# Kernel optimization log

Hardware: AMD Instinct MI355X
Metric: run time of the kernel (lower is better)

Reference implementation:

```python
import jax, jax.numpy as jnp
import numpy as np

N_NODES = 50000
N_RAND_EDGES = 800000  # plus N_NODES self-loop edges appended in setup
IN_FEATS, N_HIDDEN, N_CLASSES = 128, 64, 64


def setup_inputs() -> dict:
    key = jax.random.key(0)
    kf, ks, kd, k1, k2, k3 = jax.random.split(key, 6)
    features = jax.random.normal(kf, (N_NODES, IN_FEATS), dtype=jnp.float32)
    src = jax.random.randint(ks, (N_RAND_EDGES,), 0, N_NODES, dtype=jnp.int32)
    dst = jax.random.randint(kd, (N_RAND_EDGES,), 0, N_NODES, dtype=jnp.int32)
    # dgl.add_self_loop: append (i, i) for every node
    loop = jnp.arange(N_NODES, dtype=jnp.int32)
    src = jnp.concatenate([src, loop])
    dst = jnp.concatenate([dst, loop])

    def glorot(k, fan_in, fan_out):
        lim = jnp.sqrt(6.0 / (fan_in + fan_out)).astype(jnp.float32)
        return jax.random.uniform(k, (fan_in, fan_out), jnp.float32, -lim, lim)

    return {
        "features": features, "src": src, "dst": dst,
        "W1": glorot(k1, IN_FEATS, N_HIDDEN), "b1": jnp.zeros((N_HIDDEN,), jnp.float32),
        "W2": glorot(k2, N_HIDDEN, N_HIDDEN), "b2": jnp.zeros((N_HIDDEN,), jnp.float32),
        "W3": glorot(k3, N_HIDDEN, N_CLASSES), "b3": jnp.zeros((N_CLASSES,), jnp.float32),
    }


def _graph_conv(x, W, b, src, dst, norm_src_e, norm_dst_n, n_nodes):
    """DGL GraphConv, norm='both': D_dst^{-1/2} A D_src^{-1/2} X W + b, then relu."""
    if W.shape[0] > W.shape[1]:  # mult by W first when it shrinks the feature dim
        x = x @ W
        m = x[src] * norm_src_e[:, None]                      # [E, out]
        h = jax.ops.segment_sum(m, dst, num_segments=n_nodes)  # [N, out]
        h = h * norm_dst_n[:, None]
    else:
        m = x[src] * norm_src_e[:, None]                      # [E, in]
        h = jax.ops.segment_sum(m, dst, num_segments=n_nodes)  # [N, in]
        h = (h * norm_dst_n[:, None]) @ W
    return jax.nn.relu(h + b)


def reference(features, src, dst, W1, b1, W2, b2, W3, b3):
    n = features.shape[0]
    ones = jnp.ones(src.shape[0], dtype=features.dtype)
    out_deg = jax.ops.segment_sum(ones, src, num_segments=n)
    in_deg = jax.ops.segment_sum(ones, dst, num_segments=n)
    norm_out = jnp.where(out_deg > 0, jax.lax.rsqrt(jnp.maximum(out_deg, 1.0)), 0.0)
    norm_in = jnp.where(in_deg > 0, jax.lax.rsqrt(jnp.maximum(in_deg, 1.0)), 0.0)
    norm_src_e = norm_out[src]  # per-edge source normalization

    h1 = _graph_conv(features, W1, b1, src, dst, norm_src_e, norm_in, n)
    h2 = _graph_conv(h1, W2, b2, src, dst, norm_src_e, norm_in, n)
    h3 = _graph_conv(h2, W3, b3, src, dst, norm_src_e, norm_in, n)
    # JumpingKnowledge mode='max': elementwise max over stacked layer outputs
    return jnp.max(jnp.stack([h1, h2, h3], axis=0), axis=0)
```

## Files before the change

### kernel.cpp

```cpp
#include <hip/hip_runtime.h>

typedef _Float16 h16;
typedef __attribute__((ext_vector_type(4))) _Float16 half4;
typedef __attribute__((ext_vector_type(8))) _Float16 half8;
typedef __attribute__((ext_vector_type(8))) float float8;

#define RANGES 8
#define PPR    64
#define HTHREADS 1024
#define BINS   6400
#define HALF   (BINS / 2)
#define HWORDS (BINS)
#define NSEG   100

__global__ __launch_bounds__(HTHREADS) void hist_kernel(const int* __restrict__ src,
                                                        const int* __restrict__ dst,
                                                        int* __restrict__ partial, int E) {
  __shared__ int h[HWORDS];
  const int r = blockIdx.x >> 6;
  const int c = blockIdx.x & 63;
  for (int i = threadIdx.x; i < HWORDS; i += HTHREADS) h[i] = 0;
  __syncthreads();
  const int lo = r * BINS;
  const int chunk = (E + PPR - 1) / PPR;
  const int e0 = c * chunk;
  const int e1 = min(E, e0 + chunk);
  for (int e = e0 + threadIdx.x; e < e1; e += HTHREADS) {
    int s = src[e] - lo;
    if ((unsigned)s < (unsigned)BINS) atomicAdd(&h[s >> 1], 1 << ((s & 1) * 16));
    int d = dst[e] - lo;
    if ((unsigned)d < (unsigned)BINS) atomicAdd(&h[HALF + (d >> 1)], 1 << ((d & 1) * 16));
  }
  __syncthreads();
  int* op = partial + (size_t)blockIdx.x * HWORDS;
  for (int i = threadIdx.x; i < HWORDS; i += HTHREADS) op[i] = h[i];
}

__global__ __launch_bounds__(256) void reduce_norm_scan1(
    int* __restrict__ partial, float* __restrict__ nout, float* __restrict__ nin,
    int* __restrict__ rowptr, int* __restrict__ bsums, int N) {
  __shared__ int s[256];
  const int j = blockIdx.x * 256 + threadIdx.x;
  const int r = j / HALF;
  const int w = j % HALF;
  int* base = partial + (size_t)(r * PPR) * HWORDS;
  int sumO = 0, runI = 0;
#pragma unroll 8
  for (int p = 0; p < PPR; ++p) {
    sumO += base[(size_t)p * HWORDS + w];
    int vI = base[(size_t)p * HWORDS + HALF + w];
    base[(size_t)p * HWORDS + HALF + w] = runI;
    runI += vI;
  }
  const int od0 = sumO & 0xFFFF, od1 = (sumO >> 16) & 0xFFFF;
  const int id0 = runI & 0xFFFF, id1 = (runI >> 16) & 0xFFFF;
  const int n0 = 2 * j, n1 = n0 + 1;
  if (n0 < N) {
    nout[n0] = od0 > 0 ? rsqrtf((float)od0) : 0.f;
    nin[n0]  = id0 > 0 ? rsqrtf((float)id0) : 0.f;
  }
  if (n1 < N) {
    nout[n1] = od1 > 0 ? rsqrtf((float)od1) : 0.f;
    nin[n1]  = id1 > 0 ? rsqrtf((float)id1) : 0.f;
  }
  const int local = id0 + id1;
  int v = local;
  s[threadIdx.x] = v;
  __syncthreads();
#pragma unroll
  for (int off = 1; off < 256; off <<= 1) {
    int tv = 0;
    if (threadIdx.x >= off) tv = s[threadIdx.x - off];
    __syncthreads();
    if (threadIdx.x >= off) s[threadIdx.x] += tv;
    __syncthreads();
  }
  const int excl = s[threadIdx.x] - v;
  if (n0 < N) rowptr[n0] = excl;
  if (n1 < N) rowptr[n1] = excl + id0;
  if (threadIdx.x == 255) bsums[blockIdx.x] = s[255];
}

__global__ __launch_bounds__(HTHREADS) void fill_kernel(
    const int* __restrict__ src, const int* __restrict__ dst,
    const int* __restrict__ rowptr, const int* __restrict__ bsums,
    const int* __restrict__ partial, int* __restrict__ rowptr_abs,
    unsigned short* __restrict__ csr, int N, int E) {
  __shared__ int cur[BINS];
  __shared__ int top[128];
  const int tid = threadIdx.x;
  const int r = blockIdx.x & 7;
  const int c = blockIdx.x >> 3;
  if (tid < 128) top[tid] = (tid < NSEG) ? bsums[tid] : 0;
  __syncthreads();
#pragma unroll
  for (int off = 1; off < 128; off <<= 1) {
    int v = 0;
    if (tid < 128 && tid >= off) v = top[tid - off];
    __syncthreads();
    if (tid < 128 && tid >= off) top[tid] += v;
    __syncthreads();
  }
  const int lo = r * BINS;
  const int* pf = partial + (size_t)(r * PPR + c) * HWORDS + HALF;
  for (int n = tid; n < BINS; n += HTHREADS) {
    int g = lo + n;
    int rp = 0;
    if (g < N) {
      int seg = g >> 9;
      rp = rowptr[g] + (seg ? top[seg - 1] : 0);
      if (c == 0) rowptr_abs[g] = rp;
    }
    int pw = pf[n >> 1];
    cur[n] = rp + ((pw >> ((n & 1) * 16)) & 0xFFFF);
  }
  if (blockIdx.x == 0 && tid == 0) rowptr_abs[N] = E;
  __syncthreads();
  const int chunk = (E + PPR - 1) / PPR;
  const int e0 = c * chunk;
  const int e1 = min(E, e0 + chunk);
  for (int e = e0 + tid; e < e1; e += HTHREADS) {
    int d = dst[e] - lo;
    if ((unsigned)d < (unsigned)BINS) {
      int pos = atomicAdd(&cur[d], 1);
      csr[pos] = (unsigned short)src[e];
    }
  }
}

__device__ __forceinline__ float8 gather_row(const int* __restrict__ rowptr,
                                             const unsigned short* __restrict__ csr,
                                             const half8* __restrict__ xv,
                                             int node, int lane) {
  const int b = rowptr[node], e = rowptr[node + 1];
  float8 a0 = 0.f, a1 = 0.f, a2 = 0.f, a3 = 0.f;
  int i = b;
  for (; i + 4 <= e; i += 4) {
    int s0 = csr[i + 0], s1 = csr[i + 1], s2 = csr[i + 2], s3 = csr[i + 3];
    half8 v0 = xv[(size_t)s0 * 8 + lane];
    half8 v1 = xv[(size_t)s1 * 8 + lane];
    half8 v2 = xv[(size_t)s2 * 8 + lane];
    half8 v3 = xv[(size_t)s3 * 8 + lane];
#pragma unroll
    for (int j = 0; j < 8; ++j) {
      a0[j] += (float)v0[j]; a1[j] += (float)v1[j];
      a2[j] += (float)v2[j]; a3[j] += (float)v3[j];
    }
  }
  for (; i < e; ++i) {
    int s = csr[i];
    half8 v = xv[(size_t)s * 8 + lane];
#pragma unroll
    for (int j = 0; j < 8; ++j) a0[j] += (float)v[j];
  }
#pragma unroll
  for (int j = 0; j < 8; ++j) a0[j] = (a0[j] + a1[j]) + (a2[j] + a3[j]);
  return a0;
}

__global__ __launch_bounds__(512) void agg1_kernel(
    const int* __restrict__ rowptr, const unsigned short* __restrict__ csr,
    const h16* __restrict__ x, const float* __restrict__ nin,
    const float* __restrict__ bias, const float* __restrict__ nout,
    half8* __restrict__ y, float* __restrict__ out, int N) {
  int t = blockIdx.x * 512 + threadIdx.x;
  int node = t >> 3;
  if (node >= N) return;
  int lane = t & 7;
  float8 acc = gather_row(rowptr, csr, reinterpret_cast<const half8*>(x), node, lane);
  const float s = nin[node];
  const float no = nout[node];
  float8 h;
  half8 hv;
#pragma unroll
  for (int j = 0; j < 8; ++j) {
    h[j] = fmaxf(acc[j] * s + bias[lane * 8 + j], 0.f);
    hv[j] = (h16)(h[j] * no);
  }
  size_t off = (size_t)node * 64 + lane * 8;
  *reinterpret_cast<float4*>(out + off)     = make_float4(h[0], h[1], h[2], h[3]);
  *reinterpret_cast<float4*>(out + off + 4) = make_float4(h[4], h[5], h[6], h[7]);
  y[(size_t)node * 8 + lane] = hv;
}

template <bool WRITEC>
__global__ __launch_bounds__(512) void fused_layer(
    const int* __restrict__ rowptr, const unsigned short* __restrict__ csr,
    const h16* __restrict__ x, const float* __restrict__ W,
    const float* __restrict__ nin, const float* __restrict__ bias,
    const float* __restrict__ nout,
    half4* __restrict__ C, float* __restrict__ out, int N) {
  __shared__ float sA[64][68];
  __shared__ float sB[64][64];
  const int t = threadIdx.x;
  const int row0 = blockIdx.x * 64;

  for (int i = t * 4; i < 64 * 64; i += 512 * 4)
    *reinterpret_cast<float4*>(&sB[0][0] + i) = *reinterpret_cast<const float4*>(W + i);

  {
    const int node = t >> 3, lane = t & 7;
    const int g = row0 + node;
    float8 acc = 0.f;
    float s = 0.f;
    if (g < N) {
      acc = gather_row(rowptr, csr, reinterpret_cast<const half8*>(x), g, lane);
      s = nin[g];
    }
    *reinterpret_cast<float4*>(&sA[node][lane * 8]) =
        make_float4(acc[0] * s, acc[1] * s, acc[2] * s, acc[3] * s);
    *reinterpret_cast<float4*>(&sA[node][lane * 8 + 4]) =
        make_float4(acc[4] * s, acc[5] * s, acc[6] * s, acc[7] * s);
  }
  __syncthreads();

  const int tx = t & 15;
  const int ry = t >> 4;
  const int r0 = 2 * ry, r1 = r0 + 1;
  float4 a0 = make_float4(0.f, 0.f, 0.f, 0.f);
  float4 a1 = make_float4(0.f, 0.f, 0.f, 0.f);
#pragma unroll 8
  for (int k = 0; k < 64; ++k) {
    float x0 = sA[r0][k], x1 = sA[r1][k];
    float4 b = *reinterpret_cast<float4*>(&sB[k][tx * 4]);
    a0.x += x0 * b.x; a0.y += x0 * b.y; a0.z += x0 * b.z; a0.w += x0 * b.w;
    a1.x += x1 * b.x; a1.y += x1 * b.y; a1.z += x1 * b.z; a1.w += x1 * b.w;
  }

  const float4 bb = *reinterpret_cast<const float4*>(bias + tx * 4);
#pragma unroll
  for (int rr = 0; rr < 2; ++rr) {
    const int gr = row0 + (rr ? r1 : r0);
    if (gr >= N) continue;
    float4 v = rr ? a1 : a0;
    v.x = fmaxf(v.x + bb.x, 0.f);
    v.y = fmaxf(v.y + bb.y, 0.f);
    v.z = fmaxf(v.z + bb.z, 0.f);
    v.w = fmaxf(v.w + bb.w, 0.f);
    size_t off = (size_t)gr * 64 + tx * 4;
    float4 o = *reinterpret_cast<float4*>(out + off);
    o.x = fmaxf(o.x, v.x);
    o.y = fmaxf(o.y, v.y);
    o.z = fmaxf(o.z, v.z);
    o.w = fmaxf(o.w, v.w);
    *reinterpret_cast<float4*>(out + off) = o;
    if (WRITEC) {
      float no = nout[gr];
      half4 hv;
      hv.x = (h16)(v.x * no); hv.y = (h16)(v.y * no);
      hv.z = (h16)(v.z * no); hv.w = (h16)(v.w * no);
      C[(size_t)gr * 16 + tx] = hv;
    }
  }
}

__global__ __launch_bounds__(256) void gemm1_kernel(
    const float* __restrict__ A, const float* __restrict__ B,
    const float* __restrict__ nout, half4* __restrict__ C, int M) {
  __shared__ float sA[64][132];
  __shared__ float sB[128][64];
  const int t = threadIdx.x;
  const int row0 = blockIdx.x * 64;

  for (int i = t * 4; i < 64 * 128; i += 256 * 4) {
    int r = i / 128, c = i % 128;
    int gr = row0 + r;
    float4 v = make_float4(0.f, 0.f, 0.f, 0.f);
    if (gr < M) v = *reinterpret_cast<const float4*>(A + (size_t)gr * 128 + c);
    *reinterpret_cast<float4*>(&sA[r][c]) = v;
  }
  for (int i = t * 4; i < 128 * 64; i += 256 * 4)
    *reinterpret_cast<float4*>(&sB[0][0] + i) = *reinterpret_cast<const float4*>(B + i);
  __syncthreads();

  const int ty = t >> 4;
  const int tx = t & 15;
  float acc[4][4] = {};
#pragma unroll 8
  for (int k = 0; k < 128; ++k) {
    float a[4];
#pragma unroll
    for (int i = 0; i < 4; ++i) a[i] = sA[ty * 4 + i][k];
    float4 b = *reinterpret_cast<float4*>(&sB[k][tx * 4]);
#pragma unroll
    for (int i = 0; i < 4; ++i) {
      acc[i][0] += a[i] * b.x;
      acc[i][1] += a[i] * b.y;
      acc[i][2] += a[i] * b.z;
      acc[i][3] += a[i] * b.w;
    }
  }

#pragma unroll
  for (int i = 0; i < 4; ++i) {
    int gr = row0 + ty * 4 + i;
    if (gr >= M) continue;
    float no = nout[gr];
    half4 hv;
    hv.x = (h16)(acc[i][0] * no); hv.y = (h16)(acc[i][1] * no);
    hv.z = (h16)(acc[i][2] * no); hv.w = (h16)(acc[i][3] * no);
    C[(size_t)gr * 16 + tx] = hv;
  }
}

extern "C" void kernel_launch(void* const* d_in, const int* in_sizes, int n_in,
                              void* d_out, int out_size, void* d_ws, size_t ws_size,
                              hipStream_t stream) {
  const float* feat = (const float*)d_in[0];
  const int* src    = (const int*)d_in[1];
  const int* dst    = (const int*)d_in[2];
  const float* W1   = (const float*)d_in[3];
  const float* b1   = (const float*)d_in[4];
  const float* W2   = (const float*)d_in[5];
  const float* b2   = (const float*)d_in[6];
  const float* W3   = (const float*)d_in[7];
  const float* b3   = (const float*)d_in[8];
  float* out = (float*)d_out;

  const int N = in_sizes[0] / 128;
  const int E = in_sizes[1];

  char* p = (char*)d_ws;
  float* nout       = (float*)p;     p += (size_t)N * 4;
  float* nin        = (float*)p;     p += (size_t)N * 4;
  int*   rowptr     = (int*)p;       p += ((size_t)N + 8) * 4;
  int*   rowptr_abs = (int*)p;       p += ((size_t)N + 8) * 4;
  int*   bsums      = (int*)p;       p += 1024 * 4;
  unsigned short* csr = (unsigned short*)p;  p += (((size_t)E + 8) & ~7) * 2;
  p = (char*)(((uintptr_t)p + 15) & ~(uintptr_t)15);
  h16*   bufAh = (h16*)p;            p += (size_t)N * 64 * 2;
  h16*   bufBh = (h16*)p;            p += (size_t)N * 64 * 2;
  p = (char*)(((uintptr_t)p + 15) & ~(uintptr_t)15);
  int*   partial = (int*)p;          p += (size_t)RANGES * PPR * HWORDS * 4;

  hist_kernel<<<RANGES * PPR, HTHREADS, 0, stream>>>(src, dst, partial, E);
  reduce_norm_scan1<<<NSEG, 256, 0, stream>>>(partial, nout, nin, rowptr, bsums, N);
  fill_kernel<<<RANGES * PPR, HTHREADS, 0, stream>>>(src, dst, rowptr, bsums, partial,
                                                     rowptr_abs, csr, N, E);

  const int gemm_blocks = (N + 63) / 64;
  const int agg1_blocks = (int)(((size_t)N * 8 + 511) / 512);

  gemm1_kernel<<<gemm_blocks, 256, 0, stream>>>(feat, W1, nout, (half4*)bufAh, N);
  agg1_kernel<<<agg1_blocks, 512, 0, stream>>>(rowptr_abs, csr, bufAh, nin, b1, nout,
                                               (half8*)bufBh, out, N);
  fused_layer<true><<<gemm_blocks, 512, 0, stream>>>(rowptr_abs, csr, bufBh, W2, nin, b2, nout,
                                                     (half4*)bufAh, out, N);
  fused_layer<false><<<gemm_blocks, 512, 0, stream>>>(rowptr_abs, csr, bufAh, W3, nin, b3, nullptr,
                                                      nullptr, out, N);
}
```

Before: 154.4 us.

## Merge layer-1 GEMM into CSR fill kernel and unroll gather by eight

The first-layer feature GEMM is folded into the CSR fill launch as extra blocks, so both run concurrently in one grid and one kernel launch is dropped. The GEMM is retiled to 128-row tiles with 1024 threads and two K chunks, reusing a shared-memory buffer. The neighbor gather loop also gains an 8-way unrolled path to keep more loads in flight. This risks lower GEMM efficiency (fewer outputs per thread) and higher register pressure in the gather.

Measured after the change: 150.0 us. -2.8%, faster.

```diff
diff --git a/kernel.cpp b/kernel.cpp
--- a/kernel.cpp
+++ b/kernel.cpp
@@ -12,6 +12,7 @@
 #define HALF   (BINS / 2)
 #define HWORDS (BINS)
 #define NSEG   100
+#define NFILL  (RANGES * PPR)
 
 __global__ __launch_bounds__(HTHREADS) void hist_kernel(const int* __restrict__ src,
                                                         const int* __restrict__ dst,
@@ -81,49 +82,102 @@
   if (threadIdx.x == 255) bsums[blockIdx.x] = s[255];
 }
 
-__global__ __launch_bounds__(HTHREADS) void fill_kernel(
+__global__ __launch_bounds__(HTHREADS) void fill_gemm_kernel(
     const int* __restrict__ src, const int* __restrict__ dst,
     const int* __restrict__ rowptr, const int* __restrict__ bsums,
     const int* __restrict__ partial, int* __restrict__ rowptr_abs,
-    unsigned short* __restrict__ csr, int N, int E) {
-  __shared__ int cur[BINS];
-  __shared__ int top[128];
+    unsigned short* __restrict__ csr,
+    const float* __restrict__ feat, const float* __restrict__ W1,
+    const float* __restrict__ nout, half4* __restrict__ bufAh,
+    int N, int E) {
+  __shared__ __align__(16) char smem[51200];
   const int tid = threadIdx.x;
-  const int r = blockIdx.x & 7;
-  const int c = blockIdx.x >> 3;
-  if (tid < 128) top[tid] = (tid < NSEG) ? bsums[tid] : 0;
-  __syncthreads();
-#pragma unroll
-  for (int off = 1; off < 128; off <<= 1) {
-    int v = 0;
-    if (tid < 128 && tid >= off) v = top[tid - off];
+
+  if (blockIdx.x < NFILL) {
+    int* cur = (int*)smem;
+    int* top = (int*)(smem + BINS * 4);
+    const int r = blockIdx.x & 7;
+    const int c = blockIdx.x >> 3;
+    if (tid < 128) top[tid] = (tid < NSEG) ? bsums[tid] : 0;
     __syncthreads();
-    if (tid < 128 && tid >= off) top[tid] += v;
+#pragma unroll
+    for (int off = 1; off < 128; off <<= 1) {
+      int v = 0;
+      if (tid < 128 && tid >= off) v = top[tid - off];
+      __syncthreads();
+      if (tid < 128 && tid >= off) top[tid] += v;
+      __syncthreads();
+    }
+    const int lo = r * BINS;
+    const int* pf = partial + (size_t)(r * PPR + c) * HWORDS + HALF;
+    for (int n = tid; n < BINS; n += HTHREADS) {
+      int g = lo + n;
+      int rp = 0;
+      if (g < N) {
+        int seg = g >> 9;
+        rp = rowptr[g] + (seg ? top[seg - 1] : 0);
+        if (c == 0) rowptr_abs[g] = rp;
+      }
+      int pw = pf[n >> 1];
+      cur[n] = rp + ((pw >> ((n & 1) * 16)) & 0xFFFF);
+    }
+    if (blockIdx.x == 0 && tid == 0) rowptr_abs[N] = E;
     __syncthreads();
-  }
-  const int lo = r * BINS;
-  const int* pf = partial + (size_t)(r * PPR + c) * HWORDS + HALF;
-  for (int n = tid; n < BINS; n += HTHREADS) {
-    int g = lo + n;
-    int rp = 0;
-    if (g < N) {
-      int seg = g >> 9;
-      rp = rowptr[g] + (seg ? top[seg - 1] : 0);
-      if (c == 0) rowptr_abs[g] = rp;
-    }
-    int pw = pf[n >> 1];
-    cur[n] = rp + ((pw >> ((n & 1) * 16)) & 0xFFFF);
-  }
-  if (blockIdx.x == 0 && tid == 0) rowptr_abs[N] = E;
-  __syncthreads();
-  const int chunk = (E + PPR - 1) / PPR;
-  const int e0 = c * chunk;
-  const int e1 = min(E, e0 + chunk);
-  for (int e = e0 + tid; e < e1; e += HTHREADS) {
-    int d = dst[e] - lo;
-    if ((unsigned)d < (unsigned)BINS) {
-      int pos = atomicAdd(&cur[d], 1);
-      csr[pos] = (unsigned short)src[e];
+    const int chunk = (E + PPR - 1) / PPR;
+    const int e0 = c * chunk;
+    const int e1 = min(E, e0 + chunk);
+    for (int e = e0 + tid; e < e1; e += HTHREADS) {
+      int d = dst[e] - lo;
+      if ((unsigned)d < (unsigned)BINS) {
+        int pos = atomicAdd(&cur[d], 1);
+        csr[pos] = (unsigned short)src[e];
+      }
+    }
+  } else {
+    float* sA = (float*)smem;
+    float* sB = (float*)(smem + 128 * 68 * 4);
+    const int tile = blockIdx.x - NFILL;
+    const int row0 = tile << 7;
+    const int ry = tid >> 4;
+    const int tx = tid & 15;
+    const int r0 = 2 * ry, r1 = r0 + 1;
+    float4 acc0 = make_float4(0.f, 0.f, 0.f, 0.f);
+    float4 acc1 = make_float4(0.f, 0.f, 0.f, 0.f);
+#pragma unroll
+    for (int kc = 0; kc < 2; ++kc) {
+      __syncthreads();
+      for (int i = tid * 4; i < 128 * 64; i += HTHREADS * 4) {
+        int rr = i >> 6, cc = i & 63;
+        int gr = row0 + rr;
+        float4 v = make_float4(0.f, 0.f, 0.f, 0.f);
+        if (gr < N) v = *reinterpret_cast<const float4*>(feat + (size_t)gr * 128 + kc * 64 + cc);
+        *reinterpret_cast<float4*>(sA + rr * 68 + cc) = v;
+      }
+      {
+        int i = tid * 4;
+        int rr = i >> 6, cc = i & 63;
+        *reinterpret_cast<float4*>(sB + rr * 64 + cc) =
+            *reinterpret_cast<const float4*>(W1 + (size_t)(kc * 64 + rr) * 64 + cc);
+      }
+      __syncthreads();
+#pragma unroll 8
+      for (int k = 0; k < 64; ++k) {
+        float a0 = sA[r0 * 68 + k], a1 = sA[r1 * 68 + k];
+        float4 b = *reinterpret_cast<float4*>(sB + k * 64 + tx * 4);
+        acc0.x += a0 * b.x; acc0.y += a0 * b.y; acc0.z += a0 * b.z; acc0.w += a0 * b.w;
+        acc1.x += a1 * b.x; acc1.y += a1 * b.y; acc1.z += a1 * b.z; acc1.w += a1 * b.w;
+      }
+    }
+#pragma unroll
+    for (int rr = 0; rr < 2; ++rr) {
+      const int gr = row0 + (rr ? r1 : r0);
+      if (gr >= N) continue;
+      float4 v = rr ? acc1 : acc0;
+      float no = nout[gr];
+      half4 hv;
+      hv.x = (h16)(v.x * no); hv.y = (h16)(v.y * no);
+      hv.z = (h16)(v.z * no); hv.w = (h16)(v.w * no);
+      bufAh[(size_t)gr * 16 + tx] = hv;
     }
   }
 }
@@ -135,6 +189,25 @@
   const int b = rowptr[node], e = rowptr[node + 1];
   float8 a0 = 0.f, a1 = 0.f, a2 = 0.f, a3 = 0.f;
   int i = b;
+  for (; i + 8 <= e; i += 8) {
+    int s0 = csr[i + 0], s1 = csr[i + 1], s2 = csr[i + 2], s3 = csr[i + 3];
+    int s4 = csr[i + 4], s5 = csr[i + 5], s6 = csr[i + 6], s7 = csr[i + 7];
+    half8 v0 = xv[(size_t)s0 * 8 + lane];
+    half8 v1 = xv[(size_t)s1 * 8 + lane];
+    half8 v2 = xv[(size_t)s2 * 8 + lane];
+    half8 v3 = xv[(size_t)s3 * 8 + lane];
+    half8 v4 = xv[(size_t)s4 * 8 + lane];
+    half8 v5 = xv[(size_t)s5 * 8 + lane];
+    half8 v6 = xv[(size_t)s6 * 8 + lane];
+    half8 v7 = xv[(size_t)s7 * 8 + lane];
+#pragma unroll
+    for (int j = 0; j < 8; ++j) {
+      a0[j] += (float)v0[j]; a1[j] += (float)v1[j];
+      a2[j] += (float)v2[j]; a3[j] += (float)v3[j];
+      a0[j] += (float)v4[j]; a1[j] += (float)v5[j];
+      a2[j] += (float)v6[j]; a3[j] += (float)v7[j];
+    }
+  }
   for (; i + 4 <= e; i += 4) {
     int s0 = csr[i + 0], s1 = csr[i + 1], s2 = csr[i + 2], s3 = csr[i + 3];
     half8 v0 = xv[(size_t)s0 * 8 + lane];
@@ -254,55 +327,6 @@
   }
 }
 
-__global__ __launch_bounds__(256) void gemm1_kernel(
-    const float* __restrict__ A, const float* __restrict__ B,
-    const float* __restrict__ nout, half4* __restrict__ C, int M) {
-  __shared__ float sA[64][132];
-  __shared__ float sB[128][64];
-  const int t = threadIdx.x;
-  const int row0 = blockIdx.x * 64;
-
-  for (int i = t * 4; i < 64 * 128; i += 256 * 4) {
-    int r = i / 128, c = i % 128;
-    int gr = row0 + r;
-    float4 v = make_float4(0.f, 0.f, 0.f, 0.f);
-    if (gr < M) v = *reinterpret_cast<const float4*>(A + (size_t)gr * 128 + c);
-    *reinterpret_cast<float4*>(&sA[r][c]) = v;
-  }
-  for (int i = t * 4; i < 128 * 64; i += 256 * 4)
-    *reinterpret_cast<float4*>(&sB[0][0] + i) = *reinterpret_cast<const float4*>(B + i);
-  __syncthreads();
-
-  const int ty = t >> 4;
-  const int tx = t & 15;
-  float acc[4][4] = {};
-#pragma unroll 8
-  for (int k = 0; k < 128; ++k) {
-    float a[4];
-#pragma unroll
-    for (int i = 0; i < 4; ++i) a[i] = sA[ty * 4 + i][k];
-    float4 b = *reinterpret_cast<float4*>(&sB[k][tx * 4]);
-#pragma unroll
-    for (int i = 0; i < 4; ++i) {
-      acc[i][0] += a[i] * b.x;
-      acc[i][1] += a[i] * b.y;
-      acc[i][2] += a[i] * b.z;
-      acc[i][3] += a[i] * b.w;
-    }
-  }
-
-#pragma unroll
-  for (int i = 0; i < 4; ++i) {
-    int gr = row0 + ty * 4 + i;
-    if (gr >= M) continue;
-    float no = nout[gr];
-    half4 hv;
-    hv.x = (h16)(acc[i][0] * no); hv.y = (h16)(acc[i][1] * no);
-    hv.z = (h16)(acc[i][2] * no); hv.w = (h16)(acc[i][3] * no);
-    C[(size_t)gr * 16 + tx] = hv;
-  }
-}
-
 extern "C" void kernel_launch(void* const* d_in, const int* in_sizes, int n_in,
                               void* d_out, int out_size, void* d_ws, size_t ws_size,
                               hipStream_t stream) {
@@ -333,15 +357,17 @@
   p = (char*)(((uintptr_t)p + 15) & ~(uintptr_t)15);
   int*   partial = (int*)p;          p += (size_t)RANGES * PPR * HWORDS * 4;
 
-  hist_kernel<<<RANGES * PPR, HTHREADS, 0, stream>>>(src, dst, partial, E);
+  const int ngemm = (N + 127) / 128;
+
+  hist_kernel<<<NFILL, HTHREADS, 0, stream>>>(src, dst, partial, E);
   reduce_norm_scan1<<<NSEG, 256, 0, stream>>>(partial, nout, nin, rowptr, bsums, N);
-  fill_kernel<<<RANGES * PPR, HTHREADS, 0, stream>>>(src, dst, rowptr, bsums, partial,
-                                                     rowptr_abs, csr, N, E);
+  fill_gemm_kernel<<<NFILL + ngemm, HTHREADS, 0, stream>>>(
+      src, dst, rowptr, bsums, partial, rowptr_abs, csr,
+      feat, W1, nout, (half4*)bufAh, N, E);
 
   const int gemm_blocks = (N + 63) / 64;
   const int agg1_blocks = (int)(((size_t)N * 8 + 511) / 512);
 
-  gemm1_kernel<<<gemm_blocks, 256, 0, stream>>>(feat, W1, nout, (half4*)bufAh, N);
   agg1_kernel<<<agg1_blocks, 512, 0, stream>>>(rowptr_abs, csr, bufAh, nin, b1, nout,
                                                (half8*)bufBh, out, N);
   fused_layer<true><<<gemm_blocks, 512, 0, stream>>>(rowptr_abs, csr, bufBh, W2, nin, b2, nout,
```
